# Optimization experiments

Measured on AMD Instinct MI355X. Metric: run time of the kernel, lower is better.

## Reference

```python
import jax, jax.numpy as jnp
import numpy as np

T = 2048          # tokens (single-sequence prefill)
HID = 4096        # hidden_size
NH = 32           # num attention heads
NKV = 8           # num kv heads (GQA)
HD = 128          # head_dim
QKV_OUT = (NH + 2 * NKV) * HD  # 6144
THETA = 10000.0
SCALING = HD ** -0.5


def setup_inputs() -> dict:
    key = jax.random.key(0)
    ks = jax.random.split(key, 8)
    positions = jnp.arange(T, dtype=jnp.int32)
    # per-token int8 quantized hidden states (symmetric, [-127,127])
    q_act = jax.random.randint(ks[0], (T, HID), -127, 128, dtype=jnp.int32)
    # per-token dynamic activation scale
    act_scale = jax.random.uniform(ks[1], (T,), jnp.float32) * 0.01 + 0.001
    # int4 weights stored unsigned [0,15] with per-output-channel scale & zero point
    w_qkv_q = jax.random.randint(ks[2], (QKV_OUT, HID), 0, 16, dtype=jnp.int32)
    w_qkv_scale = jax.random.uniform(ks[3], (QKV_OUT,), jnp.float32) * 0.01 + 0.001
    w_qkv_zero = jax.random.uniform(ks[4], (QKV_OUT,), jnp.float32) * 2.0 + 7.0
    w_o_q = jax.random.randint(ks[5], (HID, HID), 0, 16, dtype=jnp.int32)
    w_o_scale = jax.random.uniform(ks[6], (HID,), jnp.float32) * 0.01 + 0.001
    w_o_zero = jax.random.uniform(ks[7], (HID,), jnp.float32) * 2.0 + 7.0
    return dict(positions=positions, q_act=q_act, act_scale=act_scale,
                w_qkv_q=w_qkv_q, w_qkv_scale=w_qkv_scale, w_qkv_zero=w_qkv_zero,
                w_o_q=w_o_q, w_o_scale=w_o_scale, w_o_zero=w_o_zero)


def w4a8_linear(qa_f, s_a, a_sum, qw, s_w, z_w):
    # y[t,o] = s_a[t]*s_w[o] * ( (qa @ qw^T)[t,o] - z_w[o]*sum_j qa[t,j] )
    acc = jnp.matmul(qa_f, qw.astype(jnp.float32).T)  # [T, O]
    return (s_a[:, None] * s_w[None, :]) * (acc - z_w[None, :] * a_sum[:, None])


def apply_rope(x, positions):
    # neox-style RoPE over full head_dim
    half = HD // 2
    inv_freq = THETA ** (-jnp.arange(0, half, dtype=jnp.float32) / half * 1.0)
    inv_freq = 1.0 / (THETA ** (jnp.arange(0, HD, 2, dtype=jnp.float32) / HD))
    freqs = positions.astype(jnp.float32)[:, None] * inv_freq[None, :]  # [T, HD/2]
    cos = jnp.cos(freqs)[:, None, :]
    sin = jnp.sin(freqs)[:, None, :]
    x1, x2 = x[..., :half], x[..., half:]
    return jnp.concatenate([x1 * cos - x2 * sin, x2 * cos + x1 * sin], axis=-1)


def dynamic_quant_with_sum(x):
    # per-token symmetric int8 dynamic quantization + fused sum
    s = jnp.maximum(jnp.max(jnp.abs(x), axis=-1), 1e-8) / 127.0  # [T]
    q = jnp.clip(jnp.round(x / s[:, None]), -127, 127)
    return q, s, jnp.sum(q, axis=-1)


def reference(positions, q_act, act_scale, w_qkv_q, w_qkv_scale, w_qkv_zero,
              w_o_q, w_o_scale, w_o_zero):
    qa_f = q_act.astype(jnp.float32)
    a_sum = jnp.sum(qa_f, axis=-1)  # fused activation sum
    qkv = w4a8_linear(qa_f, act_scale, a_sum, w_qkv_q, w_qkv_scale, w_qkv_zero)
    q, k, v = jnp.split(qkv, [NH * HD, NH * HD + NKV * HD], axis=-1)
    q = q.reshape(T, NH, HD)
    k = k.reshape(T, NKV, HD)
    v = v.reshape(T, NKV, HD)
    q = apply_rope(q, positions)
    k = apply_rope(k, positions)
    # GQA: repeat kv heads
    rep = NH // NKV
    k = jnp.repeat(k, rep, axis=1)  # [T, NH, HD]
    v = jnp.repeat(v, rep, axis=1)
    scores = jnp.einsum('qhd,khd->hqk', q, k) * SCALING  # [NH, T, T]
    causal = jnp.tril(jnp.ones((T, T), dtype=bool))
    scores = jnp.where(causal[None], scores, -jnp.inf)
    probs = jax.nn.softmax(scores, axis=-1)
    attn = jnp.einsum('hqk,khd->qhd', probs, v).reshape(T, NH * HD)
    # invoke_quant_fuse_sum: dynamic per-token quantization of attn output
    q2, s2, sum2 = dynamic_quant_with_sum(attn)
    out = w4a8_linear(q2, s2, sum2, w_o_q, w_o_scale, w_o_zero)
    return out
```

## Files before the change

### kernel.cpp

```cpp
#include <hip/hip_runtime.h>

#define T 2048
#define HID 4096
#define NH 32
#define NKV 8
#define HD 128
#define QKV_OUT ((NH + 2*NKV) * HD)
#define SCALING 0.08838834764831843f
#define QS2 0.12751744954f
#define DEFER_THR 10.0f
#define ROPE_C 0.20762050593046014f

typedef __attribute__((ext_vector_type(8))) short bfrag;
typedef __attribute__((ext_vector_type(4))) float ffrag;
typedef __attribute__((ext_vector_type(4))) int  ifrag;
typedef __attribute__((ext_vector_type(16))) char c16;

__device__ __forceinline__ short f2bf(float f) {
  unsigned u = __builtin_bit_cast(unsigned, f);
  u += 0x7fffu + ((u >> 16) & 1u);
  return (short)(u >> 16);
}

__device__ __forceinline__ void split2(float x, short& hi, short& lo) {
  unsigned u = __builtin_bit_cast(unsigned, x);
  unsigned uh = u + (0x7fffu + ((u >> 16) & 1u));
  hi = (short)(uh >> 16);
  float fh = __builtin_bit_cast(float, uh & 0xffff0000u);
  float r = x - fh;
  unsigned ur = __builtin_bit_cast(unsigned, r);
  ur += 0x7fffu + ((ur >> 16) & 1u);
  lo = (short)(ur >> 16);
}

__device__ __forceinline__ void gload_lds16(const void* g, void* l) {
  __builtin_amdgcn_global_load_lds(
      (const __attribute__((address_space(1))) unsigned int*)g,
      (__attribute__((address_space(3))) unsigned int*)l, 16, 0, 0);
}

__global__ __launch_bounds__(256)
void asum_conv(const int* __restrict__ qact, float* __restrict__ a_sum,
               char* __restrict__ a_i8) {
  __shared__ int red[256];
  const int t = blockIdx.x, tid = threadIdx.x;
  const int* row = qact + (size_t)t * HID + tid * 16;
  int s = 0;
  c16 o;
#pragma unroll
  for (int i = 0; i < 4; i++) {
    int4 v = *(const int4*)(row + i * 4);
    s += v.x + v.y + v.z + v.w;
    o[i*4+0] = (char)v.x; o[i*4+1] = (char)v.y;
    o[i*4+2] = (char)v.z; o[i*4+3] = (char)v.w;
  }
  *(c16*)(a_i8 + (size_t)t * HID + tid * 16) = o;
  red[tid] = s; __syncthreads();
  for (int off = 128; off > 0; off >>= 1) {
    if (tid < off) red[tid] += red[tid + off];
    __syncthreads();
  }
  if (tid == 0) a_sum[t] = (float)red[0];
}

__global__ __launch_bounds__(256)
void conv_i2c(const int* __restrict__ src, char* __restrict__ dst, int n16) {
  int idx = blockIdx.x * 256 + threadIdx.x;
  if (idx >= n16) return;
  const int4* s4 = (const int4*)src + (size_t)idx * 4;
  c16 o;
#pragma unroll
  for (int j = 0; j < 4; j++) {
    int4 v = s4[j];
    o[j*4+0] = (char)v.x; o[j*4+1] = (char)v.y;
    o[j*4+2] = (char)v.z; o[j*4+3] = (char)v.w;
  }
  *(c16*)(dst + (size_t)idx * 16) = o;
}

__global__ __launch_bounds__(256)
void gemm_i8(const char* __restrict__ A, const char* __restrict__ W,
             const float* __restrict__ s_a, const float* __restrict__ asum,
             const float* __restrict__ s_w, const float* __restrict__ z_w,
             float* __restrict__ C, int M, int N, int K) {
  __shared__ __align__(16) char As[128 * 64];
  __shared__ __align__(16) char Bs[128 * 64];
  const int tid = threadIdx.x;
  const int lane = tid & 63;
  const int quad = lane >> 4, l15 = lane & 15;
  const int wave = tid >> 6;
  const int wm = (wave >> 1) * 64, wn = (wave & 1) * 64;
  const int bm = blockIdx.y * 128, bn = blockIdx.x * 128;
  const int sr = tid >> 2, sc = (tid & 3) * 16;

  ifrag acc[4][4];
#pragma unroll
  for (int mi = 0; mi < 4; mi++)
#pragma unroll
    for (int ni = 0; ni < 4; ni++)
      acc[mi][ni] = (ifrag){0, 0, 0, 0};

  for (int k0 = 0; k0 < K; k0 += 64) {
#pragma unroll
    for (int it = 0; it < 2; it++) {
      gload_lds16(A + (size_t)(bm + it * 64 + sr) * K + k0 + sc,
                  &As[it * 4096 + wave * 1024]);
      gload_lds16(W + (size_t)(bn + it * 64 + sr) * K + k0 + sc,
                  &Bs[it * 4096 + wave * 1024]);
    }
    __syncthreads();

    ifrag af[4], bfv[4];
#pragma unroll
    for (int mi = 0; mi < 4; mi++)
      af[mi] = *(const ifrag*)&As[(wm + mi * 16 + l15) * 64 + quad * 16];
#pragma unroll
    for (int ni = 0; ni < 4; ni++)
      bfv[ni] = *(const ifrag*)&Bs[(wn + ni * 16 + l15) * 64 + quad * 16];
#pragma unroll
    for (int mi = 0; mi < 4; mi++)
#pragma unroll
      for (int ni = 0; ni < 4; ni++)
        acc[mi][ni] = __builtin_amdgcn_mfma_i32_16x16x64_i8(
            af[mi], bfv[ni], acc[mi][ni], 0, 0, 0);
    __syncthreads();
  }

#pragma unroll
  for (int mi = 0; mi < 4; mi++) {
    int row0 = bm + wm + mi * 16 + quad * 4;
#pragma unroll
    for (int r = 0; r < 4; r++) {
      int row = row0 + r;
      float sa = s_a[row], av = asum[row];
#pragma unroll
      for (int ni = 0; ni < 4; ni++) {
        int col = bn + wn + ni * 16 + l15;
        C[(size_t)row * N + col] = (sa * s_w[col]) * ((float)acc[mi][ni][r] - z_w[col] * av);
      }
    }
  }
}

__global__ __launch_bounds__(256)
void split_kv(float* __restrict__ qkv, const int* __restrict__ positions,
              short* __restrict__ Kh, short* __restrict__ Kl,
              short* __restrict__ Vth) {
  __shared__ __align__(16) short Vh_lds[128 * 72];
  const int y = blockIdx.y;
  const int t0 = blockIdx.x * 64;
  const int tid = threadIdx.x;

  if (y >= NKV) {
    const int h = y - NKV;
#pragma unroll
    for (int it = 0; it < 4; it++) {
      int c = tid + 256 * it;
      int key = c >> 4, dc = c & 15;
      float* qr = qkv + (size_t)(t0 + key) * QKV_OUT + (size_t)h * HD;
      float4 a = *(const float4*)(qr + dc * 4);
      float4 b = *(const float4*)(qr + dc * 4 + 64);
      float av[4] = {a.x, a.y, a.z, a.w};
      float bv[4] = {b.x, b.y, b.z, b.w};
      float pos = (float)positions[t0 + key];
#pragma unroll
      for (int jj = 0; jj < 4; jj++) {
        float fr = pos * exp2f(-ROPE_C * (float)(dc * 4 + jj));
        float sn, cs; sincosf(fr, &sn, &cs);
        float x1 = av[jj], x2 = bv[jj];
        av[jj] = x1 * cs - x2 * sn;
        bv[jj] = x2 * cs + x1 * sn;
      }
      *(float4*)(qr + dc * 4)      = make_float4(av[0], av[1], av[2], av[3]);
      *(float4*)(qr + dc * 4 + 64) = make_float4(bv[0], bv[1], bv[2], bv[3]);
    }
    return;
  }

  const int kvh = y;
#pragma unroll
  for (int it = 0; it < 4; it++) {
    int c = tid + 256 * it;
    int key = c >> 4, dc = c & 15;
    const int t = t0 + key;
    const float* kr = qkv + (size_t)t * QKV_OUT
                      + (size_t)NH * HD + (size_t)kvh * HD;
    float4 a = *(const float4*)(kr + dc * 4);
    float4 b = *(const float4*)(kr + dc * 4 + 64);
    float av[4] = {a.x, a.y, a.z, a.w};
    float bv[4] = {b.x, b.y, b.z, b.w};
    float pos = (float)positions[t];
    short4 ha, la, hb, lb;
    short hh, ll;
#pragma unroll
    for (int jj = 0; jj < 4; jj++) {
      float fr = pos * exp2f(-ROPE_C * (float)(dc * 4 + jj));
      float sn, cs; sincosf(fr, &sn, &cs);
      float x1 = av[jj], x2 = bv[jj];
      float r1 = x1 * cs - x2 * sn;
      float r2 = x2 * cs + x1 * sn;
      split2(r1, hh, ll); ((short*)&ha)[jj] = hh; ((short*)&la)[jj] = ll;
      split2(r2, hh, ll); ((short*)&hb)[jj] = hh; ((short*)&lb)[jj] = ll;
    }
    const int uu = ((dc >> 1) ^ t) & 7;
    const int h4 = (dc & 1) * 4;
    size_t base = (size_t)kvh * T * HD + (size_t)t * HD;
    *(short4*)(Kh + base + uu * 8 + h4) = ha;
    *(short4*)(Kl + base + uu * 8 + h4) = la;
    *(short4*)(Kh + base + (8 + uu) * 8 + h4) = hb;
    *(short4*)(Kl + base + (8 + uu) * 8 + h4) = lb;
  }
#pragma unroll
  for (int i = 0; i < 8; i++) {
    int c = tid + 256 * i;
    int key = c >> 5, dc = c & 31;
    float4 f = *(const float4*)(qkv + (size_t)(t0 + key) * QKV_OUT
                                + (size_t)(NH + NKV) * HD + (size_t)kvh * HD + dc * 4);
    Vh_lds[(dc*4+0)*72 + key] = f2bf(f.x);
    Vh_lds[(dc*4+1)*72 + key] = f2bf(f.y);
    Vh_lds[(dc*4+2)*72 + key] = f2bf(f.z);
    Vh_lds[(dc*4+3)*72 + key] = f2bf(f.w);
  }
  __syncthreads();
#pragma unroll
  for (int i = 0; i < 2; i++) {
    int c = tid + 256 * i;
    int row = c >> 2, cc = c & 3;
    int sd = (row >> 1) & 3;
    size_t o = (size_t)kvh * HD * T + (size_t)row * T + t0 + ((cc ^ sd)) * 8;
    *(bfrag*)(Vth + o) = *(const bfrag*)&Vh_lds[row * 72 + cc * 8];
  }
#pragma unroll
  for (int i = 0; i < 2; i++) {
    int c = tid + 256 * i;
    int row = c >> 2, cc = c & 3;
    int sd = (row >> 1) & 3;
    size_t o = (size_t)kvh * HD * T + (size_t)row * T + t0 + 32 + ((cc ^ sd)) * 8;
    *(bfrag*)(Vth + o) = *(const bfrag*)&Vh_lds[row * 72 + 32 + cc * 8];
  }
}

__global__ __launch_bounds__(256)
void attn_kernel(const float* __restrict__ qkv,
                 const short* __restrict__ Kh, const short* __restrict__ Kl,
                 const short* __restrict__ Vth,
                 float* __restrict__ Opart, float* __restrict__ Mp,
                 float* __restrict__ Lp, float* __restrict__ attn) {
  __shared__ __align__(16) short Ksh[32 * 128];
  __shared__ __align__(16) short Ksl[32 * 128];
  __shared__ __align__(16) short Vsh[128 * 32];
  __shared__ __align__(16) short Psh[4 * 16 * 40];

  const int kvh = blockIdx.y;
  const int qt  = 127 - (int)(blockIdx.x >> 1);
  const int half = blockIdx.x & 1;
  const int tid = threadIdx.x;
  const int lane = tid & 63;
  const int wv = tid >> 6;
  const int l15 = lane & 15, quad = lane >> 4;
  const int h = kvh * 4 + wv;
  short* Pw = Psh + wv * 16 * 40;

  const short* KhB = Kh + (size_t)kvh * T * HD;
  const short* KlB = Kl + (size_t)kvh * T * HD;
  const short* VhB = Vth + (size_t)kvh * HD * T;

  const int offK0 = (tid >> 4) * 128 + (tid & 15) * 8;
  const int offK1 = offK0 + 16 * 128;
  const int offV0 = (tid >> 2) * T + (tid & 3) * 8;
  const int offV1 = offV0 + 64 * T;
  const int wv1k = wv * 1024;

  const int sdv = (l15 >> 1) & 3;
  const int vq8 = (quad ^ sdv) * 8;
  int uuk[4];
#pragma unroll
  for (int kc = 0; kc < 4; kc++) {
    int s = 4 * kc + quad;
    uuk[kc] = ((s & 8) | ((s ^ l15) & 7)) * 8;
  }

  bfrag ones;
#pragma unroll
  for (int j = 0; j < 8; j++) ones[j] = (short)0x3f80;

  const int q0 = qt * 16;
  const int nk = (q0 >> 5) + 1;

  bfrag qh[4], ql[4];
  const float* qrow = qkv + (size_t)(q0 + l15) * QKV_OUT + (size_t)h * HD;
#pragma unroll
  for (int kc = 0; kc < 4; kc++) {
    float4 f0 = *(const float4*)(qrow + kc * 32 + quad * 8);
    float4 f1 = *(const float4*)(qrow + kc * 32 + quad * 8 + 4);
    float fv[8] = {f0.x, f0.y, f0.z, f0.w, f1.x, f1.y, f1.z, f1.w};
#pragma unroll
    for (int j = 0; j < 8; j++) {
      short hi, lo; split2(fv[j] * QS2, hi, lo);
      qh[kc][j] = hi; ql[kc][j] = lo;
    }
  }

  ffrag o[8], ol;
  ol = (ffrag){0.f, 0.f, 0.f, 0.f};
#pragma unroll
  for (int n = 0; n < 8; n++) o[n] = (ffrag){0.f, 0.f, 0.f, 0.f};
  float m_i[4] = {-1e30f, -1e30f, -1e30f, -1e30f};

  for (int kt = half; kt < nk; kt += 2) {
    const int k0 = kt << 5;
    __syncthreads();
    {
      const short* khs = KhB + (size_t)k0 * HD;
      const short* kls = KlB + (size_t)k0 * HD;
      const short* vs  = VhB + k0;
      gload_lds16(khs + offK0, (char*)Ksh + wv1k);
      gload_lds16(khs + offK1, (char*)Ksh + 4096 + wv1k);
      gload_lds16(kls + offK0, (char*)Ksl + wv1k);
      gload_lds16(kls + offK1, (char*)Ksl + 4096 + wv1k);
      gload_lds16(vs + offV0, (char*)Vsh + wv1k);
      gload_lds16(vs + offV1, (char*)Vsh + 4096 + wv1k);
    }
    __syncthreads();

    ffrag s[2];
    s[0] = (ffrag){0.f,0.f,0.f,0.f}; s[1] = (ffrag){0.f,0.f,0.f,0.f};
#pragma unroll
    for (int kc = 0; kc < 4; kc++) {
#pragma unroll
      for (int n = 0; n < 2; n++) {
        const int rb = (n * 16 + l15) * 128 + uuk[kc];
        bfrag bh = *(const bfrag*)&Ksh[rb];
        bfrag bl = *(const bfrag*)&Ksl[rb];
        s[n] = __builtin_amdgcn_mfma_f32_16x16x32_bf16(qh[kc], bh, s[n], 0,0,0);
        s[n] = __builtin_amdgcn_mfma_f32_16x16x32_bf16(qh[kc], bl, s[n], 0,0,0);
        s[n] = __builtin_amdgcn_mfma_f32_16x16x32_bf16(ql[kc], bh, s[n], 0,0,0);
      }
    }
    const bool lastkt = (kt == nk - 1);
    float sv[2][4];
#pragma unroll
    for (int n = 0; n < 2; n++)
#pragma unroll
      for (int r = 0; r < 4; r++) {
        float v = s[n][r];
        if (lastkt) {
          int key = k0 + n * 16 + l15;
          int row = q0 + quad * 4 + r;
          if (key > row) v = -1e30f;
        }
        sv[n][r] = v;
      }
    float mt[4];
    bool trig = false;
#pragma unroll
    for (int r = 0; r < 4; r++) {
      float m2 = fmaxf(sv[0][r], sv[1][r]);
      m2 = fmaxf(m2, __shfl_xor(m2, 1));
      m2 = fmaxf(m2, __shfl_xor(m2, 2));
      m2 = fmaxf(m2, __shfl_xor(m2, 4));
      m2 = fmaxf(m2, __shfl_xor(m2, 8));
      mt[r] = m2;
      trig = trig || (m2 > m_i[r] + DEFER_THR);
    }
    if (__any(trig)) {
#pragma unroll
      for (int r = 0; r < 4; r++) {
        float mn = fmaxf(m_i[r], mt[r]);
        float a = exp2f(m_i[r] - mn);
        m_i[r] = mn;
        ol[r] *= a;
#pragma unroll
        for (int n = 0; n < 8; n++) o[n][r] *= a;
      }
    }
#pragma unroll
    for (int n = 0; n < 2; n++)
#pragma unroll
      for (int r = 0; r < 4; r++) {
        float p = exp2f(sv[n][r] - m_i[r]);
        Pw[(quad*4 + r) * 40 + n*16 + l15] = f2bf(p);
      }
    bfrag ph = *(const bfrag*)&Pw[l15 * 40 + quad * 8];
    ol = __builtin_amdgcn_mfma_f32_16x16x32_bf16(ph, ones, ol, 0,0,0);
#pragma unroll
    for (int n = 0; n < 8; n++) {
      bfrag vh = *(const bfrag*)&Vsh[(n * 16 + l15) * 32 + vq8];
      o[n] = __builtin_amdgcn_mfma_f32_16x16x32_bf16(ph, vh, o[n], 0,0,0);
    }
  }

  float* dst = half ? attn : Opart;
#pragma unroll
  for (int n = 0; n < 8; n++)
#pragma unroll
    for (int r = 0; r < 4; r++) {
      int row = q0 + quad * 4 + r;
      dst[(size_t)row * HID + (size_t)h * HD + n * 16 + l15] = o[n][r];
    }
  if (l15 == 0) {
#pragma unroll
    for (int r = 0; r < 4; r++) {
      int row = q0 + quad * 4 + r;
      size_t ix = (size_t)half * NH * T + (size_t)h * T + row;
      Mp[ix] = m_i[r];
      Lp[ix] = ol[r];
    }
  }
}

__global__ __launch_bounds__(256)
void attn_combine(const float* __restrict__ Opart, const float* __restrict__ Mp,
                  const float* __restrict__ Lp, float* attn) {
  const int row = blockIdx.x, tid = threadIdx.x;
  const int h = tid >> 3;
  const float m0 = Mp[(size_t)h * T + row];
  const float m1 = Mp[(size_t)NH * T + (size_t)h * T + row];
  const float l0 = Lp[(size_t)h * T + row];
  const float l1 = Lp[(size_t)NH * T + (size_t)h * T + row];
  const float m = fmaxf(m0, m1);
  float s0 = exp2f(m0 - m), s1 = exp2f(m1 - m);
  const float inv = 1.f / (l0 * s0 + l1 * s1);
  s0 *= inv; s1 *= inv;
  const size_t base = (size_t)row * HID + (size_t)tid * 16;
  float4* dst = (float4*)(attn + base);
  const float4* p0 = (const float4*)(Opart + base);
#pragma unroll
  for (int i = 0; i < 4; i++) {
    float4 a = p0[i];
    float4 b = dst[i];
    dst[i] = make_float4(a.x * s0 + b.x * s1, a.y * s0 + b.y * s1,
                         a.z * s0 + b.z * s1, a.w * s0 + b.w * s1);
  }
}

__global__ __launch_bounds__(256)
void quant_kernel(const float* __restrict__ x, char* __restrict__ q2,
                  float* __restrict__ s2, float* __restrict__ sum2) {
  __shared__ float red[256];
  const int t = blockIdx.x, tid = threadIdx.x;
  const float* row = x + (size_t)t * HID;
  float4 v[4];
  float m = 0.f;
#pragma unroll
  for (int i = 0; i < 4; i++) {
    v[i] = *(const float4*)(row + tid * 16 + i * 4);
    m = fmaxf(m, fmaxf(fmaxf(fabsf(v[i].x), fabsf(v[i].y)),
                       fmaxf(fabsf(v[i].z), fabsf(v[i].w))));
  }
  red[tid] = m; __syncthreads();
  for (int off = 128; off > 0; off >>= 1) {
    if (tid < off) red[tid] = fmaxf(red[tid], red[tid + off]);
    __syncthreads();
  }
  float s = fmaxf(red[0], 1e-8f) / 127.f;
  __syncthreads();
  float ssum = 0.f;
  c16 o;
#pragma unroll
  for (int i = 0; i < 4; i++) {
    float q;
    q = fminf(127.f, fmaxf(-127.f, rintf(v[i].x / s))); ssum += q; o[i*4+0] = (char)(int)q;
    q = fminf(127.f, fmaxf(-127.f, rintf(v[i].y / s))); ssum += q; o[i*4+1] = (char)(int)q;
    q = fminf(127.f, fmaxf(-127.f, rintf(v[i].z / s))); ssum += q; o[i*4+2] = (char)(int)q;
    q = fminf(127.f, fmaxf(-127.f, rintf(v[i].w / s))); ssum += q; o[i*4+3] = (char)(int)q;
  }
  *(c16*)(q2 + (size_t)t * HID + tid * 16) = o;
  red[tid] = ssum; __syncthreads();
  for (int off = 128; off > 0; off >>= 1) {
    if (tid < off) red[tid] += red[tid + off];
    __syncthreads();
  }
  if (tid == 0) { s2[t] = s; sum2[t] = red[0]; }
}

extern "C" void kernel_launch(void* const* d_in, const int* in_sizes, int n_in,
                              void* d_out, int out_size, void* d_ws, size_t ws_size,
                              hipStream_t stream) {
  const int*   positions   = (const int*)d_in[0];
  const int*   q_act       = (const int*)d_in[1];
  const float* act_scale   = (const float*)d_in[2];
  const int*   w_qkv_q     = (const int*)d_in[3];
  const float* w_qkv_scale = (const float*)d_in[4];
  const float* w_qkv_zero  = (const float*)d_in[5];
  const int*   w_o_q       = (const int*)d_in[6];
  const float* w_o_scale   = (const float*)d_in[7];
  const float* w_o_zero    = (const float*)d_in[8];
  float* out = (float*)d_out;

  size_t off = 0;
  auto alloc = [&](size_t bytes) -> void* {
    void* p = (char*)d_ws + off;
    off += (bytes + 255) & ~(size_t)255;
    return p;
  };
  float* qkv   = (float*)alloc((size_t)T * QKV_OUT * 4);
  char*  act8  = (char*)alloc((size_t)T * HID);
  char*  w8    = (char*)alloc((size_t)QKV_OUT * HID);
  short* Kh    = (short*)alloc((size_t)NKV * T * HD * 2);
  short* Kl    = (short*)alloc((size_t)NKV * T * HD * 2);
  short* Vth   = (short*)alloc((size_t)NKV * T * HD * 2);
  float* a_sum = (float*)alloc(T * 4);
  float* s2    = (float*)alloc(T * 4);
  float* sum2  = (float*)alloc(T * 4);
  float* Mp    = (float*)alloc((size_t)2 * NH * T * 4);
  float* Lp    = (float*)alloc((size_t)2 * NH * T * 4);
  float* Opart = (float*)act8;
  (void)ws_size;

  asum_conv<<<T, 256, 0, stream>>>(q_act, a_sum, act8);
  conv_i2c<<<(QKV_OUT * HID / 16 + 255) / 256, 256, 0, stream>>>(
      w_qkv_q, w8, QKV_OUT * HID / 16);
  gemm_i8<<<dim3(QKV_OUT / 128, T / 128), 256, 0, stream>>>(
      act8, w8, act_scale, a_sum, w_qkv_scale, w_qkv_zero, qkv, T, QKV_OUT, HID);
  split_kv<<<dim3(T / 64, NKV + NH), 256, 0, stream>>>(qkv, positions, Kh, Kl, Vth);
  attn_kernel<<<dim3(256, NKV), 256, 0, stream>>>(
      qkv, Kh, Kl, Vth, Opart, Mp, Lp, out);
  attn_combine<<<T, 256, 0, stream>>>(Opart, Mp, Lp, out);
  conv_i2c<<<(HID * HID / 16 + 255) / 256, 256, 0, stream>>>(
      w_o_q, w8, HID * HID / 16);
  quant_kernel<<<T, 256, 0, stream>>>(out, act8, s2, sum2);
  gemm_i8<<<dim3(HID / 128, T / 128), 256, 0, stream>>>(
      act8, w8, s2, sum2, w_o_scale, w_o_zero, out, T, HID, HID);
}
```

Measured before the change: 575.3 us.

## Replace split-KV attention with paired causal tiles and double-buffered LDS

Each block now handles a long and a short query tile (qt and 127-qt), looping over all keys itself instead of splitting keys across two blocks. The separate combine kernel and its partial-result traffic are removed, and the 1/l normalisation happens in-kernel. K/V tiles are double-buffered in LDS so the next tile's loads overlap compute. The grid shrinks from 2048 to 512 blocks, which may reduce occupancy and latency hiding on a GPU with many CUs.

```diff
diff --git a/kernel.cpp b/kernel.cpp
--- a/kernel.cpp
+++ b/kernel.cpp
@@ -244,16 +244,14 @@
 void attn_kernel(const float* __restrict__ qkv,
                  const short* __restrict__ Kh, const short* __restrict__ Kl,
                  const short* __restrict__ Vth,
-                 float* __restrict__ Opart, float* __restrict__ Mp,
-                 float* __restrict__ Lp, float* __restrict__ attn) {
-  __shared__ __align__(16) short Ksh[32 * 128];
-  __shared__ __align__(16) short Ksl[32 * 128];
-  __shared__ __align__(16) short Vsh[128 * 32];
+                 float* __restrict__ attn) {
+  __shared__ __align__(16) short Ksh[2][32 * 128];
+  __shared__ __align__(16) short Ksl[2][32 * 128];
+  __shared__ __align__(16) short Vsh[2][128 * 32];
   __shared__ __align__(16) short Psh[4 * 16 * 40];
 
   const int kvh = blockIdx.y;
-  const int qt  = 127 - (int)(blockIdx.x >> 1);
-  const int half = blockIdx.x & 1;
+  const int pair = blockIdx.x;
   const int tid = threadIdx.x;
   const int lane = tid & 63;
   const int wv = tid >> 6;
@@ -271,6 +269,18 @@
   const int offV1 = offV0 + 64 * T;
   const int wv1k = wv * 1024;
 
+  auto stage = [&](int k0, int b) {
+    const short* khs = KhB + (size_t)k0 * HD;
+    const short* kls = KlB + (size_t)k0 * HD;
+    const short* vs  = VhB + k0;
+    gload_lds16(khs + offK0, (char*)&Ksh[b][0] + wv1k);
+    gload_lds16(khs + offK1, (char*)&Ksh[b][0] + 4096 + wv1k);
+    gload_lds16(kls + offK0, (char*)&Ksl[b][0] + wv1k);
+    gload_lds16(kls + offK1, (char*)&Ksl[b][0] + 4096 + wv1k);
+    gload_lds16(vs + offV0, (char*)&Vsh[b][0] + wv1k);
+    gload_lds16(vs + offV1, (char*)&Vsh[b][0] + 4096 + wv1k);
+  };
+
   const int sdv = (l15 >> 1) & 3;
   const int vq8 = (quad ^ sdv) * 8;
   int uuk[4];
@@ -284,153 +294,125 @@
 #pragma unroll
   for (int j = 0; j < 8; j++) ones[j] = (short)0x3f80;
 
-  const int q0 = qt * 16;
-  const int nk = (q0 >> 5) + 1;
-
-  bfrag qh[4], ql[4];
-  const float* qrow = qkv + (size_t)(q0 + l15) * QKV_OUT + (size_t)h * HD;
-#pragma unroll
-  for (int kc = 0; kc < 4; kc++) {
-    float4 f0 = *(const float4*)(qrow + kc * 32 + quad * 8);
-    float4 f1 = *(const float4*)(qrow + kc * 32 + quad * 8 + 4);
-    float fv[8] = {f0.x, f0.y, f0.z, f0.w, f1.x, f1.y, f1.z, f1.w};
-#pragma unroll
-    for (int j = 0; j < 8; j++) {
-      short hi, lo; split2(fv[j] * QS2, hi, lo);
-      qh[kc][j] = hi; ql[kc][j] = lo;
+  for (int pass = 0; pass < 2; pass++) {
+    const int qt = pass ? pair : 127 - pair;
+    const int q0 = qt * 16;
+    const int nk = (q0 >> 5) + 1;
+
+    bfrag qh[4], ql[4];
+    const float* qrow = qkv + (size_t)(q0 + l15) * QKV_OUT + (size_t)h * HD;
+#pragma unroll
+    for (int kc = 0; kc < 4; kc++) {
+      float4 f0 = *(const float4*)(qrow + kc * 32 + quad * 8);
+      float4 f1 = *(const float4*)(qrow + kc * 32 + quad * 8 + 4);
+      float fv[8] = {f0.x, f0.y, f0.z, f0.w, f1.x, f1.y, f1.z, f1.w};
+#pragma unroll
+      for (int j = 0; j < 8; j++) {
+        short hi, lo; split2(fv[j] * QS2, hi, lo);
+        qh[kc][j] = hi; ql[kc][j] = lo;
+      }
     }
-  }
-
-  ffrag o[8], ol;
-  ol = (ffrag){0.f, 0.f, 0.f, 0.f};
-#pragma unroll
-  for (int n = 0; n < 8; n++) o[n] = (ffrag){0.f, 0.f, 0.f, 0.f};
-  float m_i[4] = {-1e30f, -1e30f, -1e30f, -1e30f};
-
-  for (int kt = half; kt < nk; kt += 2) {
-    const int k0 = kt << 5;
-    __syncthreads();
-    {
-      const short* khs = KhB + (size_t)k0 * HD;
-      const short* kls = KlB + (size_t)k0 * HD;
-      const short* vs  = VhB + k0;
-      gload_lds16(khs + offK0, (char*)Ksh + wv1k);
-      gload_lds16(khs + offK1, (char*)Ksh + 4096 + wv1k);
-      gload_lds16(kls + offK0, (char*)Ksl + wv1k);
-      gload_lds16(kls + offK1, (char*)Ksl + 4096 + wv1k);
-      gload_lds16(vs + offV0, (char*)Vsh + wv1k);
-      gload_lds16(vs + offV1, (char*)Vsh + 4096 + wv1k);
+
+    ffrag o[8], ol;
+    ol = (ffrag){0.f, 0.f, 0.f, 0.f};
+#pragma unroll
+    for (int n = 0; n < 8; n++) o[n] = (ffrag){0.f, 0.f, 0.f, 0.f};
+    float m_i[4] = {-1e30f, -1e30f, -1e30f, -1e30f};
+
+    stage(0, 0);
+    asm volatile("s_waitcnt vmcnt(0)" ::: "memory");
+    __builtin_amdgcn_s_barrier();
+
+    int cur = 0;
+    for (int kt = 0; kt < nk; kt++) {
+      const int k0 = kt << 5;
+      if (kt + 1 < nk) stage(k0 + 32, cur ^ 1);
+
+      const short* ksh = &Ksh[cur][0];
+      const short* ksl = &Ksl[cur][0];
+      const short* vsh = &Vsh[cur][0];
+
+      ffrag s[2];
+      s[0] = (ffrag){0.f,0.f,0.f,0.f}; s[1] = (ffrag){0.f,0.f,0.f,0.f};
+#pragma unroll
+      for (int kc = 0; kc < 4; kc++) {
+#pragma unroll
+        for (int n = 0; n < 2; n++) {
+          const int rb = (n * 16 + l15) * 128 + uuk[kc];
+          bfrag bh = *(const bfrag*)&ksh[rb];
+          bfrag bl = *(const bfrag*)&ksl[rb];
+          s[n] = __builtin_amdgcn_mfma_f32_16x16x32_bf16(qh[kc], bh, s[n], 0,0,0);
+          s[n] = __builtin_amdgcn_mfma_f32_16x16x32_bf16(qh[kc], bl, s[n], 0,0,0);
+          s[n] = __builtin_amdgcn_mfma_f32_16x16x32_bf16(ql[kc], bh, s[n], 0,0,0);
+        }
+      }
+      const bool lastkt = (kt == nk - 1);
+      float sv[2][4];
+#pragma unroll
+      for (int n = 0; n < 2; n++)
+#pragma unroll
+        for (int r = 0; r < 4; r++) {
+          float v = s[n][r];
+          if (lastkt) {
+            int key = k0 + n * 16 + l15;
+            int row = q0 + quad * 4 + r;
+            if (key > row) v = -1e30f;
+          }
+          sv[n][r] = v;
+        }
+      float mt[4];
+      bool trig = false;
+#pragma unroll
+      for (int r = 0; r < 4; r++) {
+        float m2 = fmaxf(sv[0][r], sv[1][r]);
+        m2 = fmaxf(m2, __shfl_xor(m2, 1));
+        m2 = fmaxf(m2, __shfl_xor(m2, 2));
+        m2 = fmaxf(m2, __shfl_xor(m2, 4));
+        m2 = fmaxf(m2, __shfl_xor(m2, 8));
+        mt[r] = m2;
+        trig = trig || (m2 > m_i[r] + DEFER_THR);
+      }
+      if (__any(trig)) {
+#pragma unroll
+        for (int r = 0; r < 4; r++) {
+          float mn = fmaxf(m_i[r], mt[r]);
+          float a = exp2f(m_i[r] - mn);
+          m_i[r] = mn;
+          ol[r] *= a;
+#pragma unroll
+          for (int n = 0; n < 8; n++) o[n][r] *= a;
+        }
+      }
+#pragma unroll
+      for (int n = 0; n < 2; n++)
+#pragma unroll
+        for (int r = 0; r < 4; r++) {
+          float p = exp2f(sv[n][r] - m_i[r]);
+          Pw[(quad*4 + r) * 40 + n*16 + l15] = f2bf(p);
+        }
+      bfrag ph = *(const bfrag*)&Pw[l15 * 40 + quad * 8];
+      ol = __builtin_amdgcn_mfma_f32_16x16x32_bf16(ph, ones, ol, 0,0,0);
+#pragma unroll
+      for (int n = 0; n < 8; n++) {
+        bfrag vh = *(const bfrag*)&vsh[(n * 16 + l15) * 32 + vq8];
+        o[n] = __builtin_amdgcn_mfma_f32_16x16x32_bf16(ph, vh, o[n], 0,0,0);
+      }
+
+      asm volatile("s_waitcnt vmcnt(0)" ::: "memory");
+      __builtin_amdgcn_s_barrier();
+      cur ^= 1;
     }
-    __syncthreads();
-
-    ffrag s[2];
-    s[0] = (ffrag){0.f,0.f,0.f,0.f}; s[1] = (ffrag){0.f,0.f,0.f,0.f};
-#pragma unroll
-    for (int kc = 0; kc < 4; kc++) {
-#pragma unroll
-      for (int n = 0; n < 2; n++) {
-        const int rb = (n * 16 + l15) * 128 + uuk[kc];
-        bfrag bh = *(const bfrag*)&Ksh[rb];
-        bfrag bl = *(const bfrag*)&Ksl[rb];
-        s[n] = __builtin_amdgcn_mfma_f32_16x16x32_bf16(qh[kc], bh, s[n], 0,0,0);
-        s[n] = __builtin_amdgcn_mfma_f32_16x16x32_bf16(qh[kc], bl, s[n], 0,0,0);
-        s[n] = __builtin_amdgcn_mfma_f32_16x16x32_bf16(ql[kc], bh, s[n], 0,0,0);
-      }
-    }
-    const bool lastkt = (kt == nk - 1);
-    float sv[2][4];
-#pragma unroll
-    for (int n = 0; n < 2; n++)
+
+    float inv[4];
+#pragma unroll
+    for (int r = 0; r < 4; r++) inv[r] = 1.f / ol[r];
+#pragma unroll
+    for (int n = 0; n < 8; n++)
 #pragma unroll
       for (int r = 0; r < 4; r++) {
-        float v = s[n][r];
-        if (lastkt) {
-          int key = k0 + n * 16 + l15;
-          int row = q0 + quad * 4 + r;
-          if (key > row) v = -1e30f;
-        }
-        sv[n][r] = v;
-      }
-    float mt[4];
-    bool trig = false;
-#pragma unroll
-    for (int r = 0; r < 4; r++) {
-      float m2 = fmaxf(sv[0][r], sv[1][r]);
-      m2 = fmaxf(m2, __shfl_xor(m2, 1));
-      m2 = fmaxf(m2, __shfl_xor(m2, 2));
-      m2 = fmaxf(m2, __shfl_xor(m2, 4));
-      m2 = fmaxf(m2, __shfl_xor(m2, 8));
-      mt[r] = m2;
-      trig = trig || (m2 > m_i[r] + DEFER_THR);
-    }
-    if (__any(trig)) {
-#pragma unroll
-      for (int r = 0; r < 4; r++) {
-        float mn = fmaxf(m_i[r], mt[r]);
-        float a = exp2f(m_i[r] - mn);
-        m_i[r] = mn;
-        ol[r] *= a;
-#pragma unroll
-        for (int n = 0; n < 8; n++) o[n][r] *= a;
-      }
-    }
-#pragma unroll
-    for (int n = 0; n < 2; n++)
-#pragma unroll
-      for (int r = 0; r < 4; r++) {
-        float p = exp2f(sv[n][r] - m_i[r]);
-        Pw[(quad*4 + r) * 40 + n*16 + l15] = f2bf(p);
-      }
-    bfrag ph = *(const bfrag*)&Pw[l15 * 40 + quad * 8];
-    ol = __builtin_amdgcn_mfma_f32_16x16x32_bf16(ph, ones, ol, 0,0,0);
-#pragma unroll
-    for (int n = 0; n < 8; n++) {
-      bfrag vh = *(const bfrag*)&Vsh[(n * 16 + l15) * 32 + vq8];
-      o[n] = __builtin_amdgcn_mfma_f32_16x16x32_bf16(ph, vh, o[n], 0,0,0);
-    }
-  }
-
-  float* dst = half ? attn : Opart;
-#pragma unroll
-  for (int n = 0; n < 8; n++)
-#pragma unroll
-    for (int r = 0; r < 4; r++) {
-      int row = q0 + quad * 4 + r;
-      dst[(size_t)row * HID + (size_t)h * HD + n * 16 + l15] = o[n][r];
-    }
-  if (l15 == 0) {
-#pragma unroll
-    for (int r = 0; r < 4; r++) {
-      int row = q0 + quad * 4 + r;
-      size_t ix = (size_t)half * NH * T + (size_t)h * T + row;
-      Mp[ix] = m_i[r];
-      Lp[ix] = ol[r];
-    }
-  }
-}
-
-__global__ __launch_bounds__(256)
-void attn_combine(const float* __restrict__ Opart, const float* __restrict__ Mp,
-                  const float* __restrict__ Lp, float* attn) {
-  const int row = blockIdx.x, tid = threadIdx.x;
-  const int h = tid >> 3;
-  const float m0 = Mp[(size_t)h * T + row];
-  const float m1 = Mp[(size_t)NH * T + (size_t)h * T + row];
-  const float l0 = Lp[(size_t)h * T + row];
-  const float l1 = Lp[(size_t)NH * T + (size_t)h * T + row];
-  const float m = fmaxf(m0, m1);
-  float s0 = exp2f(m0 - m), s1 = exp2f(m1 - m);
-  const float inv = 1.f / (l0 * s0 + l1 * s1);
-  s0 *= inv; s1 *= inv;
-  const size_t base = (size_t)row * HID + (size_t)tid * 16;
-  float4* dst = (float4*)(attn + base);
-  const float4* p0 = (const float4*)(Opart + base);
-#pragma unroll
-  for (int i = 0; i < 4; i++) {
-    float4 a = p0[i];
-    float4 b = dst[i];
-    dst[i] = make_float4(a.x * s0 + b.x * s1, a.y * s0 + b.y * s1,
-                         a.z * s0 + b.z * s1, a.w * s0 + b.w * s1);
+        int row = q0 + quad * 4 + r;
+        attn[(size_t)row * HID + (size_t)h * HD + n * 16 + l15] = o[n][r] * inv[r];
+      }
   }
 }
 
@@ -503,9 +485,6 @@
   float* a_sum = (float*)alloc(T * 4);
   float* s2    = (float*)alloc(T * 4);
   float* sum2  = (float*)alloc(T * 4);
-  float* Mp    = (float*)alloc((size_t)2 * NH * T * 4);
-  float* Lp    = (float*)alloc((size_t)2 * NH * T * 4);
-  float* Opart = (float*)act8;
   (void)ws_size;
 
   asum_conv<<<T, 256, 0, stream>>>(q_act, a_sum, act8);
@@ -514,9 +493,7 @@
   gemm_i8<<<dim3(QKV_OUT / 128, T / 128), 256, 0, stream>>>(
       act8, w8, act_scale, a_sum, w_qkv_scale, w_qkv_zero, qkv, T, QKV_OUT, HID);
   split_kv<<<dim3(T / 64, NKV + NH), 256, 0, stream>>>(qkv, positions, Kh, Kl, Vth);
-  attn_kernel<<<dim3(256, NKV), 256, 0, stream>>>(
-      qkv, Kh, Kl, Vth, Opart, Mp, Lp, out);
-  attn_combine<<<T, 256, 0, stream>>>(Opart, Mp, Lp, out);
+  attn_kernel<<<dim3(64, NKV), 256, 0, stream>>>(qkv, Kh, Kl, Vth, out);
   conv_i2c<<<(HID * HID / 16 + 255) / 256, 256, 0, stream>>>(
       w_o_q, w8, HID * HID / 16);
   quant_kernel<<<T, 256, 0, stream>>>(out, act8, s2, sum2);
```

Measured after the change: 557.1 us. 1.03x faster.
